# Performance work log

Hardware: AMD Instinct MI355X
Metric: run time of the kernel (lower is better)

## Reference

```python
import jax, jax.numpy as jnp
import numpy as np

B, N, L, H = 8, 64, 256, 768
E = 2 * H            # 1536, concat(subj, obj)
NH = 12              # attention heads
HD = E // NH         # 128 head dim
HL = 1024            # LSTM hidden
C = 42               # num classes
SCALE = 0.02         # param scale for numerical sanity


def setup_inputs() -> dict:
    key = jax.random.key(0)
    ks = jax.random.split(key, 19)
    rn = lambda k, s: jax.random.normal(k, s, jnp.float32) * SCALE
    return {
        "hidden": jax.random.normal(ks[0], (B, N, L, H), jnp.float32),
        "entity_pair_inds": jax.random.randint(ks[1], (B, N, 2), 0, L),
        "Wkey": jax.random.uniform(ks[2], (E, E), jnp.float32) * SCALE,
        "Wque": jax.random.uniform(ks[3], (E, E), jnp.float32) * SCALE,
        "Wval": jax.random.uniform(ks[4], (E, E), jnp.float32) * SCALE,
        "in_proj_w": rn(ks[5], (3 * E, E)),
        "in_proj_b": rn(ks[6], (3 * E,)),
        "out_proj_w": rn(ks[7], (E, E)),
        "out_proj_b": rn(ks[8], (E,)),
        "Wih_f": rn(ks[9], (4 * HL, E)),
        "Whh_f": rn(ks[10], (4 * HL, HL)),
        "bih_f": rn(ks[11], (4 * HL,)),
        "bhh_f": rn(ks[12], (4 * HL,)),
        "Wih_b": rn(ks[13], (4 * HL, E)),
        "Whh_b": rn(ks[14], (4 * HL, HL)),
        "bih_b": rn(ks[15], (4 * HL,)),
        "bhh_b": rn(ks[16], (4 * HL,)),
        "out_w": rn(ks[17], (C, 2 * HL)),
        "out_b": rn(ks[18], (C,)),
    }


def _mha(q_in, k_in, v_in, in_proj_w, in_proj_b, out_proj_w, out_proj_b):
    # torch nn.MultiheadAttention, batch_first
    Wq, Wk, Wv = jnp.split(in_proj_w, 3, axis=0)
    bq, bk, bv = jnp.split(in_proj_b, 3, axis=0)
    b, n, _ = q_in.shape
    q = (q_in @ Wq.T + bq).reshape(b, n, NH, HD)
    k = (k_in @ Wk.T + bk).reshape(b, n, NH, HD)
    v = (v_in @ Wv.T + bv).reshape(b, n, NH, HD)
    scores = jnp.einsum("bnhd,bmhd->bhnm", q, k) / np.sqrt(HD).astype(np.float32)
    attn = jax.nn.softmax(scores, axis=-1)
    o = jnp.einsum("bhnm,bmhd->bnhd", attn, v).reshape(b, n, E)
    return o @ out_proj_w.T + out_proj_b


def _lstm_dir(x, Wih, Whh, bih, bhh):
    # single-direction LSTM over an unbatched sequence x: (T, E)
    def step(carry, xt):
        h, c = carry
        g = xt @ Wih.T + bih + h @ Whh.T + bhh  # (4*HL,)
        i, f, gg, o = jnp.split(g, 4)
        i, f, o = jax.nn.sigmoid(i), jax.nn.sigmoid(f), jax.nn.sigmoid(o)
        c = f * c + i * jnp.tanh(gg)
        h = o * jnp.tanh(c)
        return (h, c), h
    init = (jnp.zeros(HL, x.dtype), jnp.zeros(HL, x.dtype))
    _, hs = jax.lax.scan(step, init, x)
    return hs  # (T, HL)


def reference(hidden, entity_pair_inds, Wkey, Wque, Wval, in_proj_w, in_proj_b,
              out_proj_w, out_proj_b, Wih_f, Whh_f, bih_f, bhh_f,
              Wih_b, Whh_b, bih_b, bhh_b, out_w, out_b):
    # vectorized entity-pair gather: (B, N, 2) indices into token axis L
    idx = entity_pair_inds[:, :, :, None]                      # (B,N,2,1)
    pair = jnp.take_along_axis(hidden, idx, axis=2)            # (B,N,2,H)
    cat = pair.reshape(B, N, 2 * H)                            # (B,N,1536) = [subj; obj]
    keys = cat @ Wkey
    queries = cat @ Wque
    values = cat @ Wval
    # original calls attn(keys, queries, values) -> query=keys, key=queries, value=values
    attn_out = _mha(keys, queries, values, in_proj_w, in_proj_b, out_proj_w, out_proj_b)
    avg = jnp.sum(attn_out * cat, axis=1) / N                  # (B, E)
    # dropout is identity in eval mode
    # torch LSTM treats 2D input as unbatched sequence of length B
    hf = _lstm_dir(avg, Wih_f, Whh_f, bih_f, bhh_f)            # (B, HL)
    hb = _lstm_dir(avg[::-1], Wih_b, Whh_b, bih_b, bhh_b)[::-1]
    lstm_out = jnp.concatenate([hf, hb], axis=-1)              # (B, 2*HL)
    logits = lstm_out @ out_w.T + out_b                        # (B, C)
    return jax.nn.softmax(logits, axis=1)
```

## Files before the change

kernel.cpp:

```cpp
#include <hip/hip_runtime.h>
#include <hip/hip_bf16.h>
#include <cstdint>


typedef __attribute__((ext_vector_type(8))) short short8_t;
typedef __attribute__((ext_vector_type(4))) float f32x4_t;

__device__ __forceinline__ uint4 pack8(float4 a, float4 b) {
  union { uint4 u; __hip_bfloat16 h[8]; } pk;
  pk.h[0] = __float2bfloat16(a.x); pk.h[1] = __float2bfloat16(a.y);
  pk.h[2] = __float2bfloat16(a.z); pk.h[3] = __float2bfloat16(a.w);
  pk.h[4] = __float2bfloat16(b.x); pk.h[5] = __float2bfloat16(b.y);
  pk.h[6] = __float2bfloat16(b.z); pk.h[7] = __float2bfloat16(b.w);
  return pk.u;
}

__global__ __launch_bounds__(256) void prep_all_kernel(
    const float* __restrict__ hidden, const int* __restrict__ inds,
    const float* __restrict__ Wkey, const float* __restrict__ Wque, const float* __restrict__ Wval,
    float* __restrict__ cat, __hip_bfloat16* __restrict__ cat16,
    __hip_bfloat16* __restrict__ Wt16, float* __restrict__ avg0) {
  const int bid = blockIdx.x, tid = threadIdx.x;
  if (bid < 512) {
    if (bid < 48) avg0[bid * 256 + tid] = 0.f;
    int bn = bid;
    int i0 = inds[bn * 2 + 0], i1 = inds[bn * 2 + 1];
    const float* r0 = hidden + ((size_t)bn * 256 + i0) * 768;
    const float* r1 = hidden + ((size_t)bn * 256 + i1) * 768;
    float* c = cat + (size_t)bn * 1536;
    __hip_bfloat16* c16 = cat16 + (size_t)bn * 1536;
    for (int i = tid; i < 768; i += 256) {
      float a = r0[i], b = r1[i];
      c[i] = a; c[768 + i] = b;
      c16[i] = __float2bfloat16(a); c16[768 + i] = __float2bfloat16(b);
    }
  } else {
    int b2 = bid - 512;
    int z = b2 / 576, rem = b2 % 576, by = rem / 24, bx = rem % 24;
    const float* W = z == 0 ? Wkey : (z == 1 ? Wque : Wval);
    __hip_bfloat16* O = Wt16 + (size_t)z * 1536 * 1536;
    __shared__ float tile[64][65];
    int n0 = bx * 64, k0 = by * 64;
    int r = tid >> 2, q = tid & 3;
#pragma unroll
    for (int j = 0; j < 4; ++j) {
      float4 v = *(const float4*)(W + (size_t)(k0 + r) * 1536 + n0 + q * 16 + j * 4);
      tile[r][q * 16 + j * 4 + 0] = v.x; tile[r][q * 16 + j * 4 + 1] = v.y;
      tile[r][q * 16 + j * 4 + 2] = v.z; tile[r][q * 16 + j * 4 + 3] = v.w;
    }
    __syncthreads();
    union { uint4 u[2]; __hip_bfloat16 h[16]; } pk;
#pragma unroll
    for (int i = 0; i < 16; ++i) pk.h[i] = __float2bfloat16(tile[q * 16 + i][r]);
    __hip_bfloat16* dst = O + (size_t)(n0 + r) * 1536 + k0 + q * 16;
    *(uint4*)dst = pk.u[0];
    *(uint4*)(dst + 8) = pk.u[1];
  }
}

template <int CMODE, bool BIAS, bool PREPW>
__global__ __launch_bounds__(256) void mfma_gemm(
    const __hip_bfloat16* __restrict__ A, long As,
    const __hip_bfloat16* __restrict__ Bm, long Bs,
    const float* __restrict__ bias, long biasS,
    void* __restrict__ Cp, long Cs,
    const float* __restrict__ catp, float* __restrict__ avgp,
    const float* __restrict__ Whh_f, const float* __restrict__ Whh_b,
    __hip_bfloat16* __restrict__ whh16s,
    const float* __restrict__ ipw, const float* __restrict__ opw,
    __hip_bfloat16* __restrict__ inproj16, __hip_bfloat16* __restrict__ outproj16) {
  constexpr int K = 1536, N = 1536;
  const int bid = blockIdx.x, t = threadIdx.x;
  if (PREPW && bid >= 1152) {
    int tb = bid - 1152;
    if (tb < 1024) {
#pragma unroll
      for (int c = 0; c < 4; ++c) {
        int id = tb * 1024 + c * 256 + t;
        int lane = id & 63, half = (id >> 6) & 1, row = (id >> 7) & 4095, d = id >> 19;
        const float* W = d ? Whh_b : Whh_f;
        const float* srcp = W + (size_t)row * 1024 + half * 512 + lane;
        union { uint4 u; __hip_bfloat16 h[8]; } pk;
#pragma unroll
        for (int e = 0; e < 8; ++e) pk.h[e] = __float2bfloat16(srcp[e * 64]);
        *(uint4*)(whh16s + (size_t)id * 8) = pk.u;
      }
    } else {
      const float* src; __hip_bfloat16* dst; int base;
      if (tb < 1888) { src = ipw; dst = inproj16; base = (tb - 1024) * 1024; }
      else { src = opw; dst = outproj16; base = (tb - 1888) * 1024; }
#pragma unroll
      for (int c = 0; c < 4; ++c) {
        int i = base + c * 256 + t;
        float4 a = ((const float4*)src)[2 * i], b = ((const float4*)src)[2 * i + 1];
        *(uint4*)(dst + (size_t)i * 8) = pack8(a, b);
      }
    }
    return;
  }
  const int L = bid % 384, z = bid / 384;
  A += (size_t)z * As; Bm += (size_t)z * Bs;
  if (BIAS) bias += (size_t)z * biasS;
  __shared__ __align__(16) short Abuf[32 * 64];
  __shared__ __align__(16) short Bbuf[64 * 64];
  const int bxs = (L & 7) + 8 * ((L >> 3) % 3);
  const int bys = (L >> 3) / 3;
  const int i0 = bys * 32, j0 = bxs * 64;
  const int lane = t & 63, wave = t >> 6;
  f32x4_t acc[2] = {};

  const int rA = t >> 3, qA = t & 7;
  const char* Ag = (const char*)(A + (size_t)(i0 + rA) * K) + qA * 16;
  char* const Asw = (char*)Abuf + ((rA * 128 + qA * 16) ^ ((rA & 7) << 4));
  const int rB0 = t >> 3, qB0 = t & 7;
  const int tb1 = t + 256, rB1 = tb1 >> 3, qB1 = tb1 & 7;
  const char* Bg0 = (const char*)(Bm + (size_t)(j0 + rB0) * K) + qB0 * 16;
  const char* Bg1 = (const char*)(Bm + (size_t)(j0 + rB1) * K) + qB1 * 16;
  char* const Bsw0 = (char*)Bbuf + ((rB0 * 128 + qB0 * 16) ^ ((rB0 & 7) << 4));
  char* const Bsw1 = (char*)Bbuf + ((rB1 * 128 + qB1 * 16) ^ ((rB1 & 7) << 4));

  for (int kb = 0; kb < K * 2; kb += 128) {
    uint4 a0 = *(const uint4*)(Ag + kb);
    uint4 b0 = *(const uint4*)(Bg0 + kb);
    uint4 b1 = *(const uint4*)(Bg1 + kb);
    __syncthreads();
    *(uint4*)Asw = a0;
    *(uint4*)Bsw0 = b0; *(uint4*)Bsw1 = b1;
    __syncthreads();
#pragma unroll
    for (int ks = 0; ks < 2; ++ks) {
      short8_t af[2], bf;
#pragma unroll
      for (int mi = 0; mi < 2; ++mi) {
        int rr = mi * 16 + (lane & 15);
        int off = (rr * 128 + ks * 64 + (lane >> 4) * 16) ^ ((rr & 7) << 4);
        af[mi] = *(const short8_t*)((const char*)Abuf + off);
      }
      {
        int rr = wave * 16 + (lane & 15);
        int off = (rr * 128 + ks * 64 + (lane >> 4) * 16) ^ ((rr & 7) << 4);
        bf = *(const short8_t*)((const char*)Bbuf + off);
      }
#pragma unroll
      for (int mi = 0; mi < 2; ++mi)
        acc[mi] = __builtin_amdgcn_mfma_f32_16x16x32_bf16(af[mi], bf, acc[mi], 0, 0, 0);
    }
  }
  const int col = j0 + wave * 16 + (lane & 15);
  if (CMODE == 2) {
    const int b = bys >> 1;
    float bv = bias[col];
    float p = 0.f;
#pragma unroll
    for (int mi = 0; mi < 2; ++mi) {
      int rbase = i0 + mi * 16 + (lane >> 4) * 4;
#pragma unroll
      for (int r = 0; r < 4; ++r)
        p += (acc[mi][r] + bv) * catp[(size_t)(rbase + r) * 1536 + col];
    }
    p += __shfl_xor(p, 16);
    p += __shfl_xor(p, 32);
    if (lane < 16) atomicAdd(&avgp[(size_t)b * 1536 + col], p * (1.0f / 64.0f));
  } else {
    float bv = BIAS ? bias[col] : 0.f;
#pragma unroll
    for (int mi = 0; mi < 2; ++mi) {
      int r0 = i0 + mi * 16 + (lane >> 4) * 4;
#pragma unroll
      for (int r = 0; r < 4; ++r) {
        float val = acc[mi][r] + bv;
        if (CMODE == 1)
          ((__hip_bfloat16*)Cp)[(size_t)z * Cs + (size_t)(r0 + r) * N + col] = __float2bfloat16(val);
        else
          ((float*)Cp)[(size_t)z * Cs + (size_t)(r0 + r) * N + col] = val;
      }
    }
  }
}

__global__ __launch_bounds__(256) void attn2_kernel(
    const __hip_bfloat16* __restrict__ qkv, __hip_bfloat16* __restrict__ o) {
  __shared__ __align__(16) ushort Qs[64 * 128];
  __shared__ __align__(16) ushort Ks[64 * 128];
  __shared__ __align__(16) ushort Vt[128 * 72];
  __shared__ __align__(16) ushort Ps[64 * 72];
  __shared__ float redmax[2][64];
  __shared__ float redsum[2][64];
  const int b = blockIdx.x / 12, h = blockIdx.x % 12;
  const int tid = threadIdx.x, lane = tid & 63, wave = tid >> 6;
  const int wr = wave >> 1, wc = wave & 1;
  const size_t base = (size_t)b * 64 * 1536 + (size_t)h * 128;
  const __hip_bfloat16* qg = qkv + base;
  const __hip_bfloat16* kg = qkv + 786432 + base;
  const __hip_bfloat16* vg = qkv + 2 * 786432 + base;

  for (int s = tid; s < 1024; s += 256) {
    int row = s >> 4, q4 = s & 15;
    int q4s = (q4 & 8) | ((q4 & 7) ^ (row & 7));
    uint4 qv = *(const uint4*)(qg + (size_t)row * 1536 + q4 * 8);
    uint4 kv = *(const uint4*)(kg + (size_t)row * 1536 + q4 * 8);
    *(uint4*)&Qs[row * 128 + q4s * 8] = qv;
    *(uint4*)&Ks[row * 128 + q4s * 8] = kv;
    uint4 vv = *(const uint4*)(vg + (size_t)row * 1536 + q4 * 8);
    const ushort* ve = (const ushort*)&vv;
    int colv = (((row >> 3) ^ (q4 & 7)) << 3) | (row & 7);
#pragma unroll
    for (int e = 0; e < 8; ++e) Vt[(q4 * 8 + e) * 72 + colv] = ve[e];
  }
  __syncthreads();

  f32x4_t sacc[2][2] = {};
#pragma unroll
  for (int ks = 0; ks < 4; ++ks) {
    short8_t qf[2], kf[2];
#pragma unroll
    for (int mi = 0; mi < 2; ++mi) {
      int rr = wr * 32 + mi * 16 + (lane & 15);
      int slot = ks * 4 + (lane >> 4);
      int slot2 = (slot & 8) | ((slot & 7) ^ (rr & 7));
      qf[mi] = *(const short8_t*)&Qs[rr * 128 + slot2 * 8];
    }
#pragma unroll
    for (int ni = 0; ni < 2; ++ni) {
      int rr = wc * 32 + ni * 16 + (lane & 15);
      int slot = ks * 4 + (lane >> 4);
      int slot2 = (slot & 8) | ((slot & 7) ^ (rr & 7));
      kf[ni] = *(const short8_t*)&Ks[rr * 128 + slot2 * 8];
    }
#pragma unroll
    for (int mi = 0; mi < 2; ++mi)
#pragma unroll
      for (int ni = 0; ni < 2; ++ni)
        sacc[mi][ni] = __builtin_amdgcn_mfma_f32_16x16x32_bf16(qf[mi], kf[ni], sacc[mi][ni], 0, 0, 0);
  }

  const float scale = 0.08838834764831845f;
  float pv[2][2][4];
#pragma unroll
  for (int mi = 0; mi < 2; ++mi)
#pragma unroll
    for (int r = 0; r < 4; ++r) {
      float a0 = sacc[mi][0][r] * scale, a1 = sacc[mi][1][r] * scale;
      pv[mi][0][r] = a0; pv[mi][1][r] = a1;
      float m0 = fmaxf(a0, a1);
      m0 = fmaxf(m0, __shfl_xor(m0, 1));
      m0 = fmaxf(m0, __shfl_xor(m0, 2));
      m0 = fmaxf(m0, __shfl_xor(m0, 4));
      m0 = fmaxf(m0, __shfl_xor(m0, 8));
      if ((lane & 15) == 0) redmax[wc][wr * 32 + mi * 16 + (lane >> 4) * 4 + r] = m0;
    }
  __syncthreads();
#pragma unroll
  for (int mi = 0; mi < 2; ++mi)
#pragma unroll
    for (int r = 0; r < 4; ++r) {
      int row = wr * 32 + mi * 16 + (lane >> 4) * 4 + r;
      float gm = fmaxf(redmax[0][row], redmax[1][row]);
      float e0 = __expf(pv[mi][0][r] - gm);
      float e1 = __expf(pv[mi][1][r] - gm);
      pv[mi][0][r] = e0; pv[mi][1][r] = e1;
      float s0 = e0 + e1;
      s0 += __shfl_xor(s0, 1);
      s0 += __shfl_xor(s0, 2);
      s0 += __shfl_xor(s0, 4);
      s0 += __shfl_xor(s0, 8);
      if ((lane & 15) == 0) redsum[wc][row] = s0;
      int col0 = wc * 32 + (lane & 15);
      Ps[row * 72 + col0] = __bfloat16_as_ushort(__float2bfloat16(e0));
      Ps[row * 72 + col0 + 16] = __bfloat16_as_ushort(__float2bfloat16(e1));
    }
  __syncthreads();

  f32x4_t oacc[2][4] = {};
#pragma unroll
  for (int ks = 0; ks < 2; ++ks) {
    short8_t pf[2], vf[4];
#pragma unroll
    for (int mi = 0; mi < 2; ++mi) {
      int rr = wr * 32 + mi * 16 + (lane & 15);
      pf[mi] = *(const short8_t*)&Ps[rr * 72 + ks * 32 + (lane >> 4) * 8];
    }
#pragma unroll
    for (int ni = 0; ni < 4; ++ni) {
      int rr = wc * 64 + ni * 16 + (lane & 15);
      int mb = (ks * 4 + (lane >> 4)) ^ ((rr >> 3) & 7);
      vf[ni] = *(const short8_t*)&Vt[rr * 72 + mb * 8];
    }
#pragma unroll
    for (int mi = 0; mi < 2; ++mi)
#pragma unroll
      for (int ni = 0; ni < 4; ++ni)
        oacc[mi][ni] = __builtin_amdgcn_mfma_f32_16x16x32_bf16(pf[mi], vf[ni], oacc[mi][ni], 0, 0, 0);
  }

#pragma unroll
  for (int mi = 0; mi < 2; ++mi)
#pragma unroll
    for (int r = 0; r < 4; ++r) {
      int row = wr * 32 + mi * 16 + (lane >> 4) * 4 + r;
      float inv = 1.f / (redsum[0][row] + redsum[1][row]);
#pragma unroll
      for (int ni = 0; ni < 4; ++ni) {
        int col = wc * 64 + ni * 16 + (lane & 15);
        o[base + (size_t)row * 1536 + col] = __float2bfloat16(oacc[mi][ni][r] * inv);
      }
    }
}

__global__ __launch_bounds__(256) void lstm_pre3_kernel(
    const float* __restrict__ avg,
    const float* __restrict__ Wih_f, const float* __restrict__ bih_f, const float* __restrict__ bhh_f,
    const float* __restrict__ Wih_b, const float* __restrict__ bih_b, const float* __restrict__ bhh_b,
    float* __restrict__ xg, float* __restrict__ hstate, float* __restrict__ cstate,
    float* __restrict__ hout) {
  __shared__ float g4[4];
  const int bid = blockIdx.x, tid = threadIdx.x;
  const int wave = tid >> 6, lane = tid & 63;
  const int d = bid >> 10, u = bid & 1023;
  const int j = wave * 1024 + u;
  const float* W = d ? Wih_b : Wih_f;
  const float4* wrow = (const float4*)(W + (size_t)j * 1536);
  float4 w[6];
#pragma unroll
  for (int c = 0; c < 6; ++c) w[c] = wrow[c * 64 + lane];
  float s[8] = {};
#pragma unroll
  for (int r = 0; r < 8; ++r) {
    const float4* av = (const float4*)(avg + (size_t)r * 1536);
#pragma unroll
    for (int c = 0; c < 6; ++c) {
      float4 x = av[c * 64 + lane];
      s[r] += w[c].x * x.x + w[c].y * x.y + w[c].z * x.z + w[c].w * x.w;
    }
  }
#pragma unroll
  for (int r = 0; r < 8; ++r)
#pragma unroll
    for (int off = 32; off; off >>= 1) s[r] += __shfl_xor(s[r], off);
  const int r0 = d ? 7 : 0;
  if (lane == 0) {
    float bias = d ? (bih_b[j] + bhh_b[j]) : (bih_f[j] + bhh_f[j]);
#pragma unroll
    for (int r = 0; r < 8; ++r) xg[((size_t)d * 8 + r) * 4096 + j] = s[r] + bias;
    g4[wave] = s[r0] + bias;
  }
  __syncthreads();
  if (tid == 0) {
    float iv = 1.f / (1.f + __expf(-g4[0]));
    float ov = 1.f / (1.f + __expf(-g4[3]));
    float cn = iv * tanhf(g4[2]);
    float hn = ov * tanhf(cn);
    cstate[(size_t)d * 1024 + u] = cn;
    hstate[(size_t)(2 + d) * 1024 + u] = hn;
    hout[((size_t)d * 8 + r0) * 1024 + u] = hn;
  }
}

__global__ __launch_bounds__(256) void lstm_step2_kernel(
    const __hip_bfloat16* __restrict__ whh16s, const float* __restrict__ xg,
    float* __restrict__ hstate, float* __restrict__ cstate,
    float* __restrict__ hout, int s) {
  const int bid = blockIdx.x;
  const int d = bid >> 8, u0 = (bid & 255) * 4;
  const int tid = threadIdx.x, wave = tid >> 6, lane = tid & 63;
  const float* hread = hstate + ((size_t)(s & 1) * 2 + d) * 1024;
  float* hwrite = hstate + ((size_t)((s + 1) & 1) * 2 + d) * 1024;
  float* c = cstate + (size_t)d * 1024;
  const int r = d ? (7 - s) : s;

  float hreg[16];
#pragma unroll
  for (int cc = 0; cc < 16; ++cc) hreg[cc] = hread[cc * 64 + lane];

  __shared__ float gsm[4][4];
#pragma unroll
  for (int ui = 0; ui < 4; ++ui) {
    int row = wave * 1024 + u0 + ui;
    const uint4* wp = (const uint4*)whh16s + ((size_t)d * 4096 + row) * 128 + lane;
    uint4 w0 = wp[0];
    uint4 w1 = wp[64];
    float sacc = 0.f;
#pragma unroll
    for (int e4 = 0; e4 < 4; ++e4) {
      uint32_t u = ((const uint32_t*)&w0)[e4];
      sacc += __uint_as_float(u << 16) * hreg[2 * e4] +
              __uint_as_float(u & 0xffff0000u) * hreg[2 * e4 + 1];
    }
#pragma unroll
    for (int e4 = 0; e4 < 4; ++e4) {
      uint32_t u = ((const uint32_t*)&w1)[e4];
      sacc += __uint_as_float(u << 16) * hreg[8 + 2 * e4] +
              __uint_as_float(u & 0xffff0000u) * hreg[8 + 2 * e4 + 1];
    }
#pragma unroll
    for (int off = 32; off; off >>= 1) sacc += __shfl_xor(sacc, off);
    if (lane == 0) gsm[wave][ui] = sacc;
  }
  __syncthreads();
  if (tid < 4) {
    int u = u0 + tid;
    const float* xgr = xg + ((size_t)d * 8 + r) * 4096;
    float gi = gsm[0][tid] + xgr[u];
    float gf = gsm[1][tid] + xgr[1024 + u];
    float gg = gsm[2][tid] + xgr[2048 + u];
    float go = gsm[3][tid] + xgr[3072 + u];
    float iv = 1.f / (1.f + __expf(-gi));
    float fv = 1.f / (1.f + __expf(-gf));
    float ov = 1.f / (1.f + __expf(-go));
    float cold = c[u];
    float cn = fv * cold + iv * tanhf(gg);
    float hn = ov * tanhf(cn);
    c[u] = cn;
    hwrite[u] = hn;
    hout[((size_t)d * 8 + r) * 1024 + u] = hn;
  }
}

__global__ __launch_bounds__(256) void final_kernel(
    const float* __restrict__ hout, const float* __restrict__ out_w,
    const float* __restrict__ out_b, float* __restrict__ outp) {
  __shared__ float lo[2048];
  __shared__ float logits[64];
  const int s = blockIdx.x, tid = threadIdx.x;
  for (int i = tid; i < 1024; i += 256) {
    lo[i] = hout[(size_t)s * 1024 + i];
    lo[1024 + i] = hout[(size_t)(8 + s) * 1024 + i];
  }
  __syncthreads();
  const int wave = tid >> 6, lane = tid & 63;
  for (int cls = wave; cls < 42; cls += 4) {
    const float4* wr = (const float4*)(out_w + (size_t)cls * 2048);
    const float4* xr = (const float4*)lo;
    float acc = 0.f;
#pragma unroll
    for (int t = 0; t < 8; ++t) {
      int k4 = lane + t * 64;
      float4 w = wr[k4];
      float4 x = xr[k4];
      acc += w.x * x.x + w.y * x.y + w.z * x.z + w.w * x.w;
    }
#pragma unroll
    for (int off = 32; off; off >>= 1) acc += __shfl_xor(acc, off);
    if (lane == 0) logits[cls] = acc + out_b[cls];
  }
  __syncthreads();
  if (tid == 0) {
    float mx = -1e30f;
    for (int c2 = 0; c2 < 42; ++c2) mx = fmaxf(mx, logits[c2]);
    float sum = 0.f;
    for (int c2 = 0; c2 < 42; ++c2) {
      float e = __expf(logits[c2] - mx);
      logits[c2] = e;
      sum += e;
    }
    float inv = 1.f / sum;
    for (int c2 = 0; c2 < 42; ++c2) outp[s * 42 + c2] = logits[c2] * inv;
  }
}

extern "C" void kernel_launch(void* const* d_in, const int* in_sizes, int n_in,
                              void* d_out, int out_size, void* d_ws, size_t ws_size,
                              hipStream_t stream) {
  const float* hidden     = (const float*)d_in[0];
  const int*   inds       = (const int*)d_in[1];
  const float* Wkey       = (const float*)d_in[2];
  const float* Wque       = (const float*)d_in[3];
  const float* Wval       = (const float*)d_in[4];
  const float* in_proj_w  = (const float*)d_in[5];
  const float* in_proj_b  = (const float*)d_in[6];
  const float* out_proj_w = (const float*)d_in[7];
  const float* out_proj_b = (const float*)d_in[8];
  const float* Wih_f      = (const float*)d_in[9];
  const float* Whh_f      = (const float*)d_in[10];
  const float* bih_f      = (const float*)d_in[11];
  const float* bhh_f      = (const float*)d_in[12];
  const float* Wih_b      = (const float*)d_in[13];
  const float* Whh_b      = (const float*)d_in[14];
  const float* bih_b      = (const float*)d_in[15];
  const float* bhh_b      = (const float*)d_in[16];
  const float* out_w      = (const float*)d_in[17];
  const float* out_b      = (const float*)d_in[18];
  float* out = (float*)d_out;

  float* ws = (float*)d_ws;
  float* cat      = ws;
  float* avg      = cat + 786432;
  float* xg       = avg + 12288;
  float* hstate   = xg + 65536;
  float* cstate   = hstate + 4096;
  float* hout     = cstate + 2048;
  __hip_bfloat16* b16 = (__hip_bfloat16*)(hout + 16384);
  __hip_bfloat16* cat16     = b16;
  __hip_bfloat16* Wt16      = cat16 + 786432;
  __hip_bfloat16* inproj16  = Wt16 + 7077888;
  __hip_bfloat16* outproj16 = inproj16 + 7077888;
  __hip_bfloat16* kqv1      = outproj16 + 2359296;
  __hip_bfloat16* qkv16     = kqv1 + 2359296;
  __hip_bfloat16* ob16      = qkv16 + 2359296;
  __hip_bfloat16* whh16s    = ob16 + 786432;

  prep_all_kernel<<<2240, 256, 0, stream>>>(hidden, inds, Wkey, Wque, Wval,
                                            cat, cat16, Wt16, avg);

  mfma_gemm<1, false, true><<<3328, 256, 0, stream>>>(
      cat16, 0, Wt16, 1536L * 1536, nullptr, 0, kqv1, 786432, nullptr, nullptr,
      Whh_f, Whh_b, whh16s, in_proj_w, out_proj_w, inproj16, outproj16);
  mfma_gemm<1, true, false><<<1152, 256, 0, stream>>>(
      kqv1, 786432, inproj16, 1536L * 1536, in_proj_b, 1536, qkv16, 786432,
      nullptr, nullptr, nullptr, nullptr, nullptr, nullptr, nullptr, nullptr, nullptr);

  attn2_kernel<<<96, 256, 0, stream>>>(qkv16, ob16);

  mfma_gemm<2, true, false><<<384, 256, 0, stream>>>(
      ob16, 0, outproj16, 0, out_proj_b, 0, nullptr, 0, cat, avg,
      nullptr, nullptr, nullptr, nullptr, nullptr, nullptr, nullptr);

  lstm_pre3_kernel<<<2048, 256, 0, stream>>>(avg, Wih_f, bih_f, bhh_f, Wih_b, bih_b, bhh_b,
                                             xg, hstate, cstate, hout);

  for (int s = 1; s < 8; ++s)
    lstm_step2_kernel<<<512, 256, 0, stream>>>(whh16s, xg, hstate, cstate, hout, s);

  final_kernel<<<8, 256, 0, stream>>>(hout, out_w, out_b, out);
}
```

Baseline: 147.5 us.

## Spread weight bf16 conversions across later kernels to balance work

The fp32-to-bf16 conversions of the LSTM recurrent weights, in_proj and out_proj were all appended as extra blocks to the first GEMM launch. They are now split up: in_proj conversion stays with the first GEMM, Whh conversion rides along with the second GEMM, and out_proj conversion is done by extra blocks in the attention kernel, which alone only uses 96 blocks. Each conversion still finishes before the kernel that consumes it. The aim is to fill idle CUs in the underloaded launches and shorten the first launch, at the cost of more branching inside the kernels.

```diff
diff --git a/kernel.cpp b/kernel.cpp
--- a/kernel.cpp
+++ b/kernel.cpp
@@ -58,43 +58,39 @@
   }
 }
 
-template <int CMODE, bool BIAS, bool PREPW>
+template <int CMODE, bool BIAS, int TAIL>
 __global__ __launch_bounds__(256) void mfma_gemm(
     const __hip_bfloat16* __restrict__ A, long As,
     const __hip_bfloat16* __restrict__ Bm, long Bs,
     const float* __restrict__ bias, long biasS,
     void* __restrict__ Cp, long Cs,
     const float* __restrict__ catp, float* __restrict__ avgp,
-    const float* __restrict__ Whh_f, const float* __restrict__ Whh_b,
-    __hip_bfloat16* __restrict__ whh16s,
-    const float* __restrict__ ipw, const float* __restrict__ opw,
-    __hip_bfloat16* __restrict__ inproj16, __hip_bfloat16* __restrict__ outproj16) {
+    const float* __restrict__ tail_src_f, const float* __restrict__ tail_src_b,
+    __hip_bfloat16* __restrict__ tail_dst) {
   constexpr int K = 1536, N = 1536;
   const int bid = blockIdx.x, t = threadIdx.x;
-  if (PREPW && bid >= 1152) {
+  if (TAIL == 1 && bid >= 1152) {
     int tb = bid - 1152;
-    if (tb < 1024) {
-#pragma unroll
-      for (int c = 0; c < 4; ++c) {
-        int id = tb * 1024 + c * 256 + t;
-        int lane = id & 63, half = (id >> 6) & 1, row = (id >> 7) & 4095, d = id >> 19;
-        const float* W = d ? Whh_b : Whh_f;
-        const float* srcp = W + (size_t)row * 1024 + half * 512 + lane;
-        union { uint4 u; __hip_bfloat16 h[8]; } pk;
-#pragma unroll
-        for (int e = 0; e < 8; ++e) pk.h[e] = __float2bfloat16(srcp[e * 64]);
-        *(uint4*)(whh16s + (size_t)id * 8) = pk.u;
-      }
-    } else {
-      const float* src; __hip_bfloat16* dst; int base;
-      if (tb < 1888) { src = ipw; dst = inproj16; base = (tb - 1024) * 1024; }
-      else { src = opw; dst = outproj16; base = (tb - 1888) * 1024; }
-#pragma unroll
-      for (int c = 0; c < 4; ++c) {
-        int i = base + c * 256 + t;
-        float4 a = ((const float4*)src)[2 * i], b = ((const float4*)src)[2 * i + 1];
-        *(uint4*)(dst + (size_t)i * 8) = pack8(a, b);
-      }
+#pragma unroll
+    for (int c = 0; c < 4; ++c) {
+      int i = tb * 1024 + c * 256 + t;
+      float4 a = ((const float4*)tail_src_f)[2 * i], b = ((const float4*)tail_src_f)[2 * i + 1];
+      *(uint4*)(tail_dst + (size_t)i * 8) = pack8(a, b);
+    }
+    return;
+  }
+  if (TAIL == 2 && bid >= 1152) {
+    int tb = bid - 1152;
+#pragma unroll
+    for (int c = 0; c < 4; ++c) {
+      int id = tb * 1024 + c * 256 + t;
+      int lane = id & 63, half = (id >> 6) & 1, row = (id >> 7) & 4095, d = id >> 19;
+      const float* W = d ? tail_src_b : tail_src_f;
+      const float* srcp = W + (size_t)row * 1024 + half * 512 + lane;
+      union { uint4 u; __hip_bfloat16 h[8]; } pk;
+#pragma unroll
+      for (int e = 0; e < 8; ++e) pk.h[e] = __float2bfloat16(srcp[e * 64]);
+      *(uint4*)(tail_dst + (size_t)id * 8) = pk.u;
     }
     return;
   }
@@ -179,15 +175,27 @@
 }
 
 __global__ __launch_bounds__(256) void attn2_kernel(
-    const __hip_bfloat16* __restrict__ qkv, __hip_bfloat16* __restrict__ o) {
+    const __hip_bfloat16* __restrict__ qkv, __hip_bfloat16* __restrict__ o,
+    const float* __restrict__ opw, __hip_bfloat16* __restrict__ outproj16) {
   __shared__ __align__(16) ushort Qs[64 * 128];
   __shared__ __align__(16) ushort Ks[64 * 128];
   __shared__ __align__(16) ushort Vt[128 * 72];
   __shared__ __align__(16) ushort Ps[64 * 72];
   __shared__ float redmax[2][64];
   __shared__ float redsum[2][64];
+  const int tid = threadIdx.x;
+  if (blockIdx.x >= 96) {
+    int tb = blockIdx.x - 96;
+#pragma unroll
+    for (int c = 0; c < 4; ++c) {
+      int i = tb * 1024 + c * 256 + tid;
+      float4 a = ((const float4*)opw)[2 * i], b = ((const float4*)opw)[2 * i + 1];
+      *(uint4*)(outproj16 + (size_t)i * 8) = pack8(a, b);
+    }
+    return;
+  }
   const int b = blockIdx.x / 12, h = blockIdx.x % 12;
-  const int tid = threadIdx.x, lane = tid & 63, wave = tid >> 6;
+  const int lane = tid & 63, wave = tid >> 6;
   const int wr = wave >> 1, wc = wave & 1;
   const size_t base = (size_t)b * 64 * 1536 + (size_t)h * 128;
   const __hip_bfloat16* qg = qkv + base;
@@ -502,18 +510,18 @@
   prep_all_kernel<<<2240, 256, 0, stream>>>(hidden, inds, Wkey, Wque, Wval,
                                             cat, cat16, Wt16, avg);
 
-  mfma_gemm<1, false, true><<<3328, 256, 0, stream>>>(
+  mfma_gemm<1, false, 1><<<2016, 256, 0, stream>>>(
       cat16, 0, Wt16, 1536L * 1536, nullptr, 0, kqv1, 786432, nullptr, nullptr,
-      Whh_f, Whh_b, whh16s, in_proj_w, out_proj_w, inproj16, outproj16);
-  mfma_gemm<1, true, false><<<1152, 256, 0, stream>>>(
+      in_proj_w, nullptr, inproj16);
+  mfma_gemm<1, true, 2><<<2176, 256, 0, stream>>>(
       kqv1, 786432, inproj16, 1536L * 1536, in_proj_b, 1536, qkv16, 786432,
-      nullptr, nullptr, nullptr, nullptr, nullptr, nullptr, nullptr, nullptr, nullptr);
-
-  attn2_kernel<<<96, 256, 0, stream>>>(qkv16, ob16);
-
-  mfma_gemm<2, true, false><<<384, 256, 0, stream>>>(
+      nullptr, nullptr, Whh_f, Whh_b, whh16s);
+
+  attn2_kernel<<<384, 256, 0, stream>>>(qkv16, ob16, out_proj_w, outproj16);
+
+  mfma_gemm<2, true, 0><<<384, 256, 0, stream>>>(
       ob16, 0, outproj16, 0, out_proj_b, 0, nullptr, 0, cat, avg,
-      nullptr, nullptr, nullptr, nullptr, nullptr, nullptr, nullptr);
+      nullptr, nullptr, nullptr);
 
   lstm_pre3_kernel<<<2048, 256, 0, stream>>>(avg, Wih_f, bih_f, bhh_f, Wih_b, bih_b, bhh_b,
                                              xg, hstate, cstate, hout);
```

Result: no change. 145.6 us (median of 2 runs) (-1.3%).
